# Optimization experiments

Measured on AMD Instinct MI355X. Metric: run time of the kernel, lower is better.

Reference implementation:

```python
import jax, jax.numpy as jnp
import numpy as np

N = 100000      # nodes
E = 1600000     # directed edges (avg degree 16)
F_IN = 512      # config.input_layer
H1, D1 = 8, 8   # conv1: 8 heads x 8 dims
C_OUT = 40      # config.output_layer


def setup_inputs() -> dict:
    key = jax.random.key(0)
    ks = jax.random.split(key, 10)
    x = jax.random.normal(ks[0], (N, F_IN), dtype=jnp.float32)
    edge_index = jax.random.randint(ks[1], (2, E), 0, N, dtype=jnp.int64)
    s = 0.05
    W1 = jax.random.normal(ks[2], (F_IN, H1 * D1), dtype=jnp.float32) * s
    att_src1 = jax.random.normal(ks[3], (H1, D1), dtype=jnp.float32) * s
    att_dst1 = jax.random.normal(ks[4], (H1, D1), dtype=jnp.float32) * s
    b1 = jnp.zeros((H1 * D1,), dtype=jnp.float32)
    W2 = jax.random.normal(ks[5], (H1 * D1, C_OUT), dtype=jnp.float32) * s
    att_src2 = jax.random.normal(ks[6], (1, C_OUT), dtype=jnp.float32) * s
    att_dst2 = jax.random.normal(ks[7], (1, C_OUT), dtype=jnp.float32) * s
    b2 = jnp.zeros((C_OUT,), dtype=jnp.float32)
    return {"x": x, "edge_index": edge_index,
            "W1": W1, "att_src1": att_src1, "att_dst1": att_dst1, "b1": b1,
            "W2": W2, "att_src2": att_src2, "att_dst2": att_dst2, "b2": b2}


def _gat_conv(x, src, dst, W, a_src, a_dst, b, heads, concat):
    """PyG GATConv (eval mode: attention dropout is identity)."""
    n = x.shape[0]
    d = W.shape[1] // heads
    h = (x @ W).reshape(n, heads, d)                       # [N,H,D]
    alpha_s = jnp.einsum('nhd,hd->nh', h, a_src)           # [N,H]
    alpha_d = jnp.einsum('nhd,hd->nh', h, a_dst)
    e = jax.nn.leaky_relu(alpha_s[src] + alpha_d[dst], 0.2)  # [E,H]
    # numerically stable segment softmax over edges grouped by dst
    e = e - jax.ops.segment_max(e, dst, num_segments=n)[dst]
    ex = jnp.exp(e)
    denom = jax.ops.segment_sum(ex, dst, num_segments=n)[dst]
    alpha = ex / denom                                      # [E,H]
    msg = h[src] * alpha[:, :, None]                        # [E,H,D]
    out = jax.ops.segment_sum(msg, dst, num_segments=n)     # [N,H,D]
    out = out.reshape(n, heads * d) if concat else out.mean(axis=1)
    return out + b


def reference(x, edge_index, W1, att_src1, att_dst1, b1, W2, att_src2, att_dst2, b2):
    # add self loops (PyG GATConv default)
    loop = jnp.arange(x.shape[0], dtype=edge_index.dtype)
    src = jnp.concatenate([edge_index[0], loop])
    dst = jnp.concatenate([edge_index[1], loop])
    # dropout(p=0.6) layers are identity in eval mode
    h = jax.nn.elu(_gat_conv(x, src, dst, W1, att_src1, att_dst1, b1, H1, True))
    out = _gat_conv(h, src, dst, W2, att_src2, att_dst2, b2, 1, False)
    return jax.nn.log_softmax(out, axis=1)
```

## Files before the change

### kernel.cpp

```cpp
#include <hip/hip_runtime.h>

#define F_IN 512
#define H1   8
#define D1   8
#define C1   64
#define C2   40
#define C2P  48

#define BKT_SH   7
#define BKT_W    128
#define NBKT_MAX 1024
#define NBLK     128

using short8 = __attribute__((ext_vector_type(8))) short;
using f32x4  = __attribute__((ext_vector_type(4))) float;
using bf8v   = __attribute__((ext_vector_type(8))) __bf16;

__device__ __forceinline__ float leaky02(float x) { return x > 0.f ? x : 0.2f * x; }
__device__ __forceinline__ float bf2f(unsigned short u) {
    return __builtin_bit_cast(float, ((unsigned)u) << 16);
}
__device__ __forceinline__ unsigned short f2bf(float v) {
    return __builtin_bit_cast(unsigned short, (__bf16)v);
}
__device__ __forceinline__ short8 cvt_bf16x8(float4 a, float4 b) {
    bf8v r;
    r[0] = (__bf16)a.x; r[1] = (__bf16)a.y; r[2] = (__bf16)a.z; r[3] = (__bf16)a.w;
    r[4] = (__bf16)b.x; r[5] = (__bf16)b.y; r[6] = (__bf16)b.z; r[7] = (__bf16)b.w;
    return __builtin_bit_cast(short8, r);
}

__global__ __launch_bounds__(256) void wconv_kernel(
    const float* __restrict__ W1, const float* __restrict__ W2,
    unsigned short* __restrict__ Bt1, unsigned short* __restrict__ Bt2)
{
    int idx = blockIdx.x * 256 + threadIdx.x;
    if (idx < F_IN * C1) {
        int k = idx >> 6, c = idx & 63;
        Bt1[(size_t)c * F_IN + k] = f2bf(W1[idx]);
    } else if (idx < F_IN * C1 + C2P * 64) {
        int j = idx - F_IN * C1;
        int c = j >> 6, k = j & 63;
        float v = (c < C2) ? W2[k * C2 + c] : 0.f;
        Bt2[c * 64 + k] = f2bf(v);
    }
}

__global__ __launch_bounds__(256) void gemm1_kernel(
    const float* __restrict__ x, const unsigned short* __restrict__ Bt1,
    const float* __restrict__ a_src, const float* __restrict__ a_dst,
    unsigned short* __restrict__ h1b, float* __restrict__ as1,
    float* __restrict__ ad1, int N)
{
    const int tid  = threadIdx.x;
    const int w    = tid >> 6;
    const int lane = tid & 63;
    const int lo   = lane & 15;
    const int kg   = lane >> 4;
    const int n0   = blockIdx.x * 128 + w * 32;

    const int nA = min(n0 + lo, N - 1);
    const int nB = min(n0 + 16 + lo, N - 1);
    const float* xA = x + (size_t)nA * F_IN + kg * 8;
    const float* xB = x + (size_t)nB * F_IN + kg * 8;
    const unsigned short* bp = Bt1 + (size_t)lo * F_IN + kg * 8;

    float a_s[4], a_d[4];
    #pragma unroll
    for (int nt = 0; nt < 4; ++nt) {
        a_s[nt] = a_src[nt * 16 + lo];
        a_d[nt] = a_dst[nt * 16 + lo];
    }

    f32x4 acc[2][4];
    #pragma unroll
    for (int mt = 0; mt < 2; ++mt)
        #pragma unroll
        for (int nt = 0; nt < 4; ++nt)
            acc[mt][nt] = (f32x4){0.f, 0.f, 0.f, 0.f};

    #pragma unroll 4
    for (int s = 0; s < 16; ++s) {
        const int kb = s * 32;
        float4 a0 = *(const float4*)(xA + kb);
        float4 a1 = *(const float4*)(xA + kb + 4);
        float4 c0 = *(const float4*)(xB + kb);
        float4 c1 = *(const float4*)(xB + kb + 4);
        short8 bF[4];
        #pragma unroll
        for (int nt = 0; nt < 4; ++nt)
            bF[nt] = *(const short8*)(bp + (size_t)nt * 16 * F_IN + kb);
        short8 aF0 = cvt_bf16x8(a0, a1);
        short8 aF1 = cvt_bf16x8(c0, c1);
        #pragma unroll
        for (int nt = 0; nt < 4; ++nt) {
            acc[0][nt] = __builtin_amdgcn_mfma_f32_16x16x32_bf16(aF0, bF[nt], acc[0][nt], 0, 0, 0);
            acc[1][nt] = __builtin_amdgcn_mfma_f32_16x16x32_bf16(aF1, bF[nt], acc[1][nt], 0, 0, 0);
        }
    }

    #pragma unroll
    for (int mt = 0; mt < 2; ++mt) {
        #pragma unroll
        for (int j = 0; j < 4; ++j) {
            const int n = n0 + mt * 16 + kg * 4 + j;
            float sv[4], dv[4];
            #pragma unroll
            for (int nt = 0; nt < 4; ++nt) {
                float v = acc[mt][nt][j];
                sv[nt] = v * a_s[nt];
                dv[nt] = v * a_d[nt];
            }
            #pragma unroll
            for (int m = 1; m < 8; m <<= 1) {
                #pragma unroll
                for (int nt = 0; nt < 4; ++nt) {
                    sv[nt] += __shfl_xor(sv[nt], m);
                    dv[nt] += __shfl_xor(dv[nt], m);
                }
            }
            if (n < N) {
                #pragma unroll
                for (int nt = 0; nt < 4; ++nt)
                    h1b[(size_t)n * C1 + nt * 16 + lo] = f2bf(acc[mt][nt][j]);
                if ((lane & 7) == 0) {
                    const int h0 = (lane >> 3) & 1;
                    #pragma unroll
                    for (int nt = 0; nt < 4; ++nt) {
                        as1[n * H1 + h0 + nt * 2] = sv[nt];
                        ad1[n * H1 + h0 + nt * 2] = dv[nt];
                    }
                }
            }
        }
    }
}

__global__ __launch_bounds__(256) void bhist_kernel(
    const int* __restrict__ ei, int* __restrict__ blockhist,
    int E, int nbkt, int chunk)
{
    __shared__ int lh[NBKT_MAX];
    for (int i = threadIdx.x; i < nbkt; i += 256) lh[i] = 0;
    __syncthreads();
    const int b = blockIdx.x;
    const int beg = b * chunk;
    const int end = min(E, beg + chunk);
    for (int e = beg + threadIdx.x; e < end; e += 256)
        atomicAdd(&lh[ei[E + e] >> BKT_SH], 1);
    __syncthreads();
    for (int k = threadIdx.x; k < nbkt; k += 256)
        blockhist[k * NBLK + b] = lh[k];
}

__global__ __launch_bounds__(512) void scan1_kernel(
    const int* __restrict__ in, int* __restrict__ excl,
    int* __restrict__ bsum, int M)
{
    __shared__ int sA[512], sB[512];
    const int t = threadIdx.x;
    const int i = blockIdx.x * 512 + t;
    int v = (i < M) ? in[i] : 0;
    sA[t] = v; __syncthreads();
    int* pin = sA; int* pout = sB;
    #pragma unroll
    for (int off = 1; off < 512; off <<= 1) {
        pout[t] = pin[t] + ((t >= off) ? pin[t - off] : 0);
        __syncthreads();
        int* tmp = pin; pin = pout; pout = tmp;
    }
    if (i < M) excl[i] = pin[t] - v;
    if (t == 511) bsum[blockIdx.x] = pin[511];
}

__global__ __launch_bounds__(256) void scan2_kernel(
    int* __restrict__ bsum, int* __restrict__ bsumo, int NB)
{
    __shared__ int sA[256], sB[256];
    const int t = threadIdx.x;
    int v = (t < NB) ? bsum[t] : 0;
    sA[t] = v; __syncthreads();
    int* pin = sA; int* pout = sB;
    #pragma unroll
    for (int off = 1; off < 256; off <<= 1) {
        pout[t] = pin[t] + ((t >= off) ? pin[t - off] : 0);
        __syncthreads();
        int* tmp = pin; pin = pout; pout = tmp;
    }
    if (t < NB) bsumo[t] = pin[t] - v;
}

__global__ __launch_bounds__(512) void scan3_kernel(
    int* __restrict__ boffs, const int* __restrict__ bsumo, int M, int E)
{
    const int i = blockIdx.x * 512 + threadIdx.x;
    if (i < M) boffs[i] += bsumo[blockIdx.x];
    if (i == 0) boffs[M] = E;
}

__global__ __launch_bounds__(256) void bpart_kernel(
    const int* __restrict__ ei, const int* __restrict__ boffs,
    int2* __restrict__ ebuf, int E, int nbkt, int chunk)
{
    __shared__ int cur[NBKT_MAX];
    const int b = blockIdx.x;
    for (int k = threadIdx.x; k < nbkt; k += 256) cur[k] = boffs[k * NBLK + b];
    __syncthreads();
    const int beg = b * chunk;
    const int end = min(E, beg + chunk);
    for (int e = beg + threadIdx.x; e < end; e += 256) {
        int src = ei[e], dst = ei[E + e];
        int pos = atomicAdd(&cur[dst >> BKT_SH], 1);
        ebuf[pos] = make_int2(src, dst);
    }
}

__global__ __launch_bounds__(256) void bsort_kernel(
    const int* __restrict__ boffs, const int2* __restrict__ ebuf,
    int* __restrict__ rowptr, int* __restrict__ esrc, int N, int E)
{
    const int b = blockIdx.x;
    const int tid = threadIdx.x;
    const int base = boffs[b * NBLK];
    const int cnt  = boffs[(b + 1) * NBLK] - base;

    __shared__ int hist[BKT_W], scn[BKT_W], cur[BKT_W];
    if (tid < BKT_W) hist[tid] = 0;
    __syncthreads();
    for (int i = tid; i < cnt; i += 256)
        atomicAdd(&hist[ebuf[base + i].y & (BKT_W - 1)], 1);
    __syncthreads();
    if (tid < BKT_W) scn[tid] = hist[tid];
    __syncthreads();
    #pragma unroll
    for (int off = 1; off < BKT_W; off <<= 1) {
        int add = 0;
        if (tid < BKT_W && tid >= off) add = scn[tid - off];
        __syncthreads();
        if (tid < BKT_W) scn[tid] += add;
        __syncthreads();
    }
    if (tid < BKT_W) {
        int ex = base + scn[tid] - hist[tid];
        cur[tid] = ex;
        int n0 = b * BKT_W + tid;
        if (n0 < N) rowptr[n0] = ex;
    }
    if (b == 0 && tid == 0) rowptr[N] = E;
    __syncthreads();
    for (int i = tid; i < cnt; i += 256) {
        int2 ed = ebuf[base + i];
        int pos = atomicAdd(&cur[ed.y & (BKT_W - 1)], 1);
        esrc[pos] = ed.x;
    }
}

__global__ __launch_bounds__(256) void agg1_kernel(
    const int* __restrict__ rowptr, const int* __restrict__ esrc,
    const unsigned short* __restrict__ h1b, const float* __restrict__ as1,
    const float* __restrict__ ad1, const float* __restrict__ b1,
    unsigned short* __restrict__ h1f, int N)
{
    const int n = blockIdx.x * 4 + (threadIdx.x >> 6);
    if (n >= N) return;
    const int lane = threadIdx.x & 63;
    const int h = lane >> 3;
    const float adh = ad1[n * H1 + h];

    float acc = 0.f, den = 0.f;
    int i = rowptr[n];
    const int end = rowptr[n + 1];
    for (; i + 4 <= end; i += 4) {
        const int s0 = esrc[i], s1 = esrc[i + 1], s2 = esrc[i + 2], s3 = esrc[i + 3];
        const float v0 = bf2f(h1b[(size_t)s0 * C1 + lane]);
        const float v1 = bf2f(h1b[(size_t)s1 * C1 + lane]);
        const float v2 = bf2f(h1b[(size_t)s2 * C1 + lane]);
        const float v3 = bf2f(h1b[(size_t)s3 * C1 + lane]);
        const float a0 = as1[s0 * H1 + h], a1 = as1[s1 * H1 + h];
        const float a2 = as1[s2 * H1 + h], a3 = as1[s3 * H1 + h];
        const float e0 = __expf(leaky02(a0 + adh));
        const float e1 = __expf(leaky02(a1 + adh));
        const float e2 = __expf(leaky02(a2 + adh));
        const float e3 = __expf(leaky02(a3 + adh));
        acc += e0 * v0; acc += e1 * v1; acc += e2 * v2; acc += e3 * v3;
        den += (e0 + e1) + (e2 + e3);
    }
    for (; i < end; ++i) {
        const int src = esrc[i];
        const float v  = bf2f(h1b[(size_t)src * C1 + lane]);
        const float ex = __expf(leaky02(as1[src * H1 + h] + adh));
        acc += ex * v;
        den += ex;
    }
    {
        const float ex = __expf(leaky02(as1[n * H1 + h] + adh));
        acc += ex * bf2f(h1b[(size_t)n * C1 + lane]);
        den += ex;
    }
    float v = acc / den + b1[lane];
    v = v > 0.f ? v : __expf(v) - 1.f;
    h1f[(size_t)n * C1 + lane] = f2bf(v);
}

__global__ __launch_bounds__(256) void gemm2_kernel(
    const unsigned short* __restrict__ h1f, const unsigned short* __restrict__ Bt2,
    const float* __restrict__ a_src2, const float* __restrict__ a_dst2,
    unsigned short* __restrict__ h2b, float* __restrict__ as2,
    float* __restrict__ ad2, int N)
{
    const int tid  = threadIdx.x;
    const int w    = tid >> 6;
    const int lane = tid & 63;
    const int lo   = lane & 15;
    const int kg   = lane >> 4;
    const int n0   = blockIdx.x * 64 + w * 16;

    const int nA = min(n0 + lo, N - 1);
    const unsigned short* ap = h1f + (size_t)nA * C1 + kg * 8;

    float a_s[3], a_d[3];
    #pragma unroll
    for (int nt = 0; nt < 3; ++nt) {
        const int c = nt * 16 + lo;
        a_s[nt] = (c < C2) ? a_src2[c] : 0.f;
        a_d[nt] = (c < C2) ? a_dst2[c] : 0.f;
    }

    f32x4 acc[3];
    #pragma unroll
    for (int nt = 0; nt < 3; ++nt) acc[nt] = (f32x4){0.f, 0.f, 0.f, 0.f};

    #pragma unroll
    for (int ks = 0; ks < 2; ++ks) {
        short8 aF = *(const short8*)(ap + ks * 32);
        #pragma unroll
        for (int nt = 0; nt < 3; ++nt) {
            short8 bF = *(const short8*)(Bt2 + (nt * 16 + lo) * 64 + ks * 32 + kg * 8);
            acc[nt] = __builtin_amdgcn_mfma_f32_16x16x32_bf16(aF, bF, acc[nt], 0, 0, 0);
        }
    }

    #pragma unroll
    for (int j = 0; j < 4; ++j) {
        const int n = n0 + kg * 4 + j;
        float s = acc[0][j] * a_s[0] + acc[1][j] * a_s[1] + acc[2][j] * a_s[2];
        float d = acc[0][j] * a_d[0] + acc[1][j] * a_d[1] + acc[2][j] * a_d[2];
        #pragma unroll
        for (int m = 1; m < 16; m <<= 1) {
            s += __shfl_xor(s, m);
            d += __shfl_xor(d, m);
        }
        if (n < N) {
            #pragma unroll
            for (int nt = 0; nt < 3; ++nt) {
                const int c = nt * 16 + lo;
                if (c < C2) h2b[(size_t)n * C2 + c] = f2bf(acc[nt][j]);
            }
            if (lo == 0) { as2[n] = s; ad2[n] = d; }
        }
    }
}

__global__ __launch_bounds__(256) void agg2_kernel(
    const int* __restrict__ rowptr, const int* __restrict__ esrc,
    const unsigned short* __restrict__ h2b, const float* __restrict__ as2,
    const float* __restrict__ ad2, const float* __restrict__ b2,
    float* __restrict__ out, int N)
{
    const int n = blockIdx.x * 4 + (threadIdx.x >> 6);
    if (n >= N) return;
    const int lane = threadIdx.x & 63;
    const float adn = ad2[n];

    float acc = 0.f, den = 0.f;
    int i = rowptr[n];
    const int end = rowptr[n + 1];
    for (; i + 4 <= end; i += 4) {
        const int s0 = esrc[i], s1 = esrc[i + 1], s2 = esrc[i + 2], s3 = esrc[i + 3];
        float v0 = 0.f, v1 = 0.f, v2 = 0.f, v3 = 0.f;
        if (lane < C2) {
            v0 = bf2f(h2b[(size_t)s0 * C2 + lane]);
            v1 = bf2f(h2b[(size_t)s1 * C2 + lane]);
            v2 = bf2f(h2b[(size_t)s2 * C2 + lane]);
            v3 = bf2f(h2b[(size_t)s3 * C2 + lane]);
        }
        const float a0 = as2[s0], a1 = as2[s1], a2 = as2[s2], a3 = as2[s3];
        const float e0 = __expf(leaky02(a0 + adn));
        const float e1 = __expf(leaky02(a1 + adn));
        const float e2 = __expf(leaky02(a2 + adn));
        const float e3 = __expf(leaky02(a3 + adn));
        acc += e0 * v0; acc += e1 * v1; acc += e2 * v2; acc += e3 * v3;
        den += (e0 + e1) + (e2 + e3);
    }
    for (; i < end; ++i) {
        const int src = esrc[i];
        float v = (lane < C2) ? bf2f(h2b[(size_t)src * C2 + lane]) : 0.f;
        const float ex = __expf(leaky02(as2[src] + adn));
        acc += ex * v;
        den += ex;
    }
    {
        const float ex = __expf(leaky02(as2[n] + adn));
        if (lane < C2) acc += ex * bf2f(h2b[(size_t)n * C2 + lane]);
        den += ex;
    }
    float v = (lane < C2) ? (acc / den + b2[lane]) : -1e30f;
    float m = v;
    #pragma unroll
    for (int s = 1; s < 64; s <<= 1) m = fmaxf(m, __shfl_xor(m, s));
    float e2x = (lane < C2) ? __expf(v - m) : 0.f;
    #pragma unroll
    for (int s = 1; s < 64; s <<= 1) e2x += __shfl_xor(e2x, s);
    float lse = __logf(e2x);
    if (lane < C2) out[(size_t)n * C2 + lane] = v - m - lse;
}

extern "C" void kernel_launch(void* const* d_in, const int* in_sizes, int n_in,
                              void* d_out, int out_size, void* d_ws, size_t ws_size,
                              hipStream_t stream)
{
    const float* x    = (const float*)d_in[0];
    const int*   ei   = (const int*)  d_in[1];
    const float* W1   = (const float*)d_in[2];
    const float* as1w = (const float*)d_in[3];
    const float* ad1w = (const float*)d_in[4];
    const float* b1   = (const float*)d_in[5];
    const float* W2   = (const float*)d_in[6];
    const float* as2w = (const float*)d_in[7];
    const float* ad2w = (const float*)d_in[8];
    const float* b2   = (const float*)d_in[9];

    const int N = in_sizes[0] / F_IN;
    const int E = in_sizes[1] / 2;
    const int nbkt = (N + BKT_W - 1) >> BKT_SH;
    const int M    = nbkt * NBLK;
    const int chunk = (E + NBLK - 1) / NBLK;

    char* base = (char*)d_ws;
    auto carve = [&](size_t bytes) -> void* {
        void* p = (void*)base;
        base += (bytes + 255) & ~(size_t)255;
        return p;
    };
    unsigned short* h1b = (unsigned short*)carve((size_t)N * C1 * 2);
    unsigned short* h1f = (unsigned short*)carve((size_t)N * C1 * 2);
    float* as1    = (float*)carve((size_t)N * H1 * 4);
    float* ad1    = (float*)carve((size_t)N * H1 * 4);
    unsigned short* h2b = (unsigned short*)carve((size_t)N * C2 * 2);
    float* as2    = (float*)carve((size_t)N * 4);
    float* ad2    = (float*)carve((size_t)N * 4);
    int*   rowptr = (int*)carve((size_t)(N + 1) * 4);
    int*   esrc   = (int*)carve((size_t)E * 4);
    int*   boffs  = (int*)carve((size_t)(M + 1) * 4);
    int*   bsum   = (int*)carve(256 * 4);
    int*   bsumo  = (int*)carve(256 * 4);
    unsigned short* Bt1 = (unsigned short*)carve((size_t)F_IN * C1 * 2);
    unsigned short* Bt2 = (unsigned short*)carve((size_t)C2P * 64 * 2);

    int2* ebuf = (int2*)h1f;

    const int NB = (M + 511) / 512;

    wconv_kernel<<<(F_IN * C1 + C2P * 64 + 255) / 256, 256, 0, stream>>>(W1, W2, Bt1, Bt2);

    bhist_kernel<<<NBLK, 256, 0, stream>>>(ei, boffs, E, nbkt, chunk);
    scan1_kernel<<<NB, 512, 0, stream>>>(boffs, boffs, bsum, M);
    scan2_kernel<<<1, 256, 0, stream>>>(bsum, bsumo, NB);
    scan3_kernel<<<NB, 512, 0, stream>>>(boffs, bsumo, M, E);
    bpart_kernel<<<NBLK, 256, 0, stream>>>(ei, boffs, ebuf, E, nbkt, chunk);
    bsort_kernel<<<nbkt, 256, 0, stream>>>(boffs, ebuf, rowptr, esrc, N, E);

    gemm1_kernel<<<(N + 127) / 128, 256, 0, stream>>>(x, Bt1, as1w, ad1w, h1b, as1, ad1, N);
    agg1_kernel<<<(N + 3) / 4, 256, 0, stream>>>(rowptr, esrc, h1b, as1, ad1, b1, h1f, N);
    gemm2_kernel<<<(N + 63) / 64, 256, 0, stream>>>(h1f, Bt2, as2w, ad2w, h2b, as2, ad2, N);
    agg2_kernel<<<(N + 3) / 4, 256, 0, stream>>>(rowptr, esrc, h2b, as2, ad2, b2,
                                                 (float*)d_out, N);
}
```

Baseline: 336.0 us.

## Fold scan3 into consumers, pack edge buffer, prefetch next edge indices

Removes the scan3 launch by adding each block-sum offset where bpart and bsort read boffs, with the last bucket's end taken from E. Packs each (src, low dst bits) edge pair into one 32-bit word instead of an int2, halving ebuf traffic; this assumes src << 7 fits in 32 bits, which holds for N=100000. The aggregation loops in agg1 and agg2 now load the next four esrc indices before the current group's exp/accumulate work, to hide the index-load latency. Prefetching past the unrolled range reads up to four esrc entries beyond the row end, which stays in bounds except possibly at the end of the array.

```diff
diff --git a/kernel.cpp b/kernel.cpp
--- a/kernel.cpp
+++ b/kernel.cpp
@@ -190,45 +190,49 @@
     if (t < NB) bsumo[t] = pin[t] - v;
 }
 
-__global__ __launch_bounds__(512) void scan3_kernel(
-    int* __restrict__ boffs, const int* __restrict__ bsumo, int M, int E)
-{
-    const int i = blockIdx.x * 512 + threadIdx.x;
-    if (i < M) boffs[i] += bsumo[blockIdx.x];
-    if (i == 0) boffs[M] = E;
-}
-
 __global__ __launch_bounds__(256) void bpart_kernel(
     const int* __restrict__ ei, const int* __restrict__ boffs,
-    int2* __restrict__ ebuf, int E, int nbkt, int chunk)
+    const int* __restrict__ bsumo, int* __restrict__ ebuf,
+    int E, int nbkt, int chunk)
 {
     __shared__ int cur[NBKT_MAX];
     const int b = blockIdx.x;
-    for (int k = threadIdx.x; k < nbkt; k += 256) cur[k] = boffs[k * NBLK + b];
+    for (int k = threadIdx.x; k < nbkt; k += 256) {
+        const int idx = k * NBLK + b;
+        cur[k] = boffs[idx] + bsumo[idx >> 9];
+    }
     __syncthreads();
     const int beg = b * chunk;
     const int end = min(E, beg + chunk);
     for (int e = beg + threadIdx.x; e < end; e += 256) {
         int src = ei[e], dst = ei[E + e];
         int pos = atomicAdd(&cur[dst >> BKT_SH], 1);
-        ebuf[pos] = make_int2(src, dst);
+        ebuf[pos] = (src << BKT_SH) | (dst & (BKT_W - 1));
     }
 }
 
 __global__ __launch_bounds__(256) void bsort_kernel(
-    const int* __restrict__ boffs, const int2* __restrict__ ebuf,
-    int* __restrict__ rowptr, int* __restrict__ esrc, int N, int E)
+    const int* __restrict__ boffs, const int* __restrict__ bsumo,
+    const int* __restrict__ ebuf, int* __restrict__ rowptr,
+    int* __restrict__ esrc, int N, int E, int nbkt)
 {
     const int b = blockIdx.x;
     const int tid = threadIdx.x;
-    const int base = boffs[b * NBLK];
-    const int cnt  = boffs[(b + 1) * NBLK] - base;
+    const int i0 = b * NBLK;
+    const int base = boffs[i0] + bsumo[i0 >> 9];
+    int nxt;
+    if (b == nbkt - 1) nxt = E;
+    else {
+        const int i1 = (b + 1) * NBLK;
+        nxt = boffs[i1] + bsumo[i1 >> 9];
+    }
+    const int cnt = nxt - base;
 
     __shared__ int hist[BKT_W], scn[BKT_W], cur[BKT_W];
     if (tid < BKT_W) hist[tid] = 0;
     __syncthreads();
     for (int i = tid; i < cnt; i += 256)
-        atomicAdd(&hist[ebuf[base + i].y & (BKT_W - 1)], 1);
+        atomicAdd(&hist[ebuf[base + i] & (BKT_W - 1)], 1);
     __syncthreads();
     if (tid < BKT_W) scn[tid] = hist[tid];
     __syncthreads();
@@ -249,9 +253,9 @@
     if (b == 0 && tid == 0) rowptr[N] = E;
     __syncthreads();
     for (int i = tid; i < cnt; i += 256) {
-        int2 ed = ebuf[base + i];
-        int pos = atomicAdd(&cur[ed.y & (BKT_W - 1)], 1);
-        esrc[pos] = ed.x;
+        int p = ebuf[base + i];
+        int pos = atomicAdd(&cur[p & (BKT_W - 1)], 1);
+        esrc[pos] = (unsigned)p >> BKT_SH;
     }
 }
 
@@ -270,20 +274,24 @@
     float acc = 0.f, den = 0.f;
     int i = rowptr[n];
     const int end = rowptr[n + 1];
-    for (; i + 4 <= end; i += 4) {
-        const int s0 = esrc[i], s1 = esrc[i + 1], s2 = esrc[i + 2], s3 = esrc[i + 3];
+    int s0, s1, s2, s3;
+    if (i + 4 <= end) { s0 = esrc[i]; s1 = esrc[i+1]; s2 = esrc[i+2]; s3 = esrc[i+3]; }
+    for (; i + 4 <= end; ) {
         const float v0 = bf2f(h1b[(size_t)s0 * C1 + lane]);
         const float v1 = bf2f(h1b[(size_t)s1 * C1 + lane]);
         const float v2 = bf2f(h1b[(size_t)s2 * C1 + lane]);
         const float v3 = bf2f(h1b[(size_t)s3 * C1 + lane]);
         const float a0 = as1[s0 * H1 + h], a1 = as1[s1 * H1 + h];
         const float a2 = as1[s2 * H1 + h], a3 = as1[s3 * H1 + h];
+        i += 4;
+        const int t0 = esrc[i], t1 = esrc[i+1], t2 = esrc[i+2], t3 = esrc[i+3];
         const float e0 = __expf(leaky02(a0 + adh));
         const float e1 = __expf(leaky02(a1 + adh));
         const float e2 = __expf(leaky02(a2 + adh));
         const float e3 = __expf(leaky02(a3 + adh));
         acc += e0 * v0; acc += e1 * v1; acc += e2 * v2; acc += e3 * v3;
         den += (e0 + e1) + (e2 + e3);
+        s0 = t0; s1 = t1; s2 = t2; s3 = t3;
     }
     for (; i < end; ++i) {
         const int src = esrc[i];
@@ -375,8 +383,9 @@
     float acc = 0.f, den = 0.f;
     int i = rowptr[n];
     const int end = rowptr[n + 1];
-    for (; i + 4 <= end; i += 4) {
-        const int s0 = esrc[i], s1 = esrc[i + 1], s2 = esrc[i + 2], s3 = esrc[i + 3];
+    int s0, s1, s2, s3;
+    if (i + 4 <= end) { s0 = esrc[i]; s1 = esrc[i+1]; s2 = esrc[i+2]; s3 = esrc[i+3]; }
+    for (; i + 4 <= end; ) {
         float v0 = 0.f, v1 = 0.f, v2 = 0.f, v3 = 0.f;
         if (lane < C2) {
             v0 = bf2f(h2b[(size_t)s0 * C2 + lane]);
@@ -385,12 +394,15 @@
             v3 = bf2f(h2b[(size_t)s3 * C2 + lane]);
         }
         const float a0 = as2[s0], a1 = as2[s1], a2 = as2[s2], a3 = as2[s3];
+        i += 4;
+        const int t0 = esrc[i], t1 = esrc[i+1], t2 = esrc[i+2], t3 = esrc[i+3];
         const float e0 = __expf(leaky02(a0 + adn));
         const float e1 = __expf(leaky02(a1 + adn));
         const float e2 = __expf(leaky02(a2 + adn));
         const float e3 = __expf(leaky02(a3 + adn));
         acc += e0 * v0; acc += e1 * v1; acc += e2 * v2; acc += e3 * v3;
         den += (e0 + e1) + (e2 + e3);
+        s0 = t0; s1 = t1; s2 = t2; s3 = t3;
     }
     for (; i < end; ++i) {
         const int src = esrc[i];
@@ -457,7 +469,7 @@
     unsigned short* Bt1 = (unsigned short*)carve((size_t)F_IN * C1 * 2);
     unsigned short* Bt2 = (unsigned short*)carve((size_t)C2P * 64 * 2);
 
-    int2* ebuf = (int2*)h1f;
+    int* ebuf = (int*)h1f;
 
     const int NB = (M + 511) / 512;
 
@@ -466,9 +478,8 @@
     bhist_kernel<<<NBLK, 256, 0, stream>>>(ei, boffs, E, nbkt, chunk);
     scan1_kernel<<<NB, 512, 0, stream>>>(boffs, boffs, bsum, M);
     scan2_kernel<<<1, 256, 0, stream>>>(bsum, bsumo, NB);
-    scan3_kernel<<<NB, 512, 0, stream>>>(boffs, bsumo, M, E);
-    bpart_kernel<<<NBLK, 256, 0, stream>>>(ei, boffs, ebuf, E, nbkt, chunk);
-    bsort_kernel<<<nbkt, 256, 0, stream>>>(boffs, ebuf, rowptr, esrc, N, E);
+    bpart_kernel<<<NBLK, 256, 0, stream>>>(ei, boffs, bsumo, ebuf, E, nbkt, chunk);
+    bsort_kernel<<<nbkt, 256, 0, stream>>>(boffs, bsumo, ebuf, rowptr, esrc, N, E, nbkt);
 
     gemm1_kernel<<<(N + 127) / 128, 256, 0, stream>>>(x, Bt1, as1w, ad1w, h1b, as1, ad1, N);
     agg1_kernel<<<(N + 3) / 4, 256, 0, stream>>>(rowptr, esrc, h1b, as1, ad1, b1, h1f, N);
```

New measurement: 334.7 us. About the same (-0.4%).
